# Performance work log

Measured on AMD Instinct MI355X. Metric: run time of the kernel, lower is better.

Reference implementation:

```python
import jax, jax.numpy as jnp
import numpy as np
from jax import lax

COND, PRED, DH, NOUT = 64, 32, 128, 1
M, LQ, N, LR = 8, 256, 64, 512


def setup_inputs() -> dict:
    key = jax.random.key(0)
    ks = jax.random.split(key, 8)
    g = lambda k, sh, s=0.05: jax.random.normal(k, sh, jnp.float32) * s
    return {
        "query": jax.random.normal(ks[0], (M, LQ), jnp.float32),
        "ref": jax.random.normal(ks[1], (N, LR), jnp.float32),
        "q_weight": g(ks[2], (DH, 1, COND)),
        "q_bias": jnp.zeros((DH,), jnp.float32),
        "k_weight": g(ks[3], (DH, 1, COND)),
        "k_bias": jnp.zeros((DH,), jnp.float32),
        "v_weight": g(ks[4], (DH, 1, PRED), 0.1),
        "v_bias": jnp.zeros((DH,), jnp.float32),
        "m_weight": jnp.full((NOUT, 1, COND), 1.0 / COND, jnp.float32),
        "m_bias": jnp.zeros((NOUT,), jnp.float32),
        "o_weight": g(ks[5], (NOUT * PRED, DH), 0.1),
        "o_bias": jnp.zeros((NOUT * PRED,), jnp.float32),
        "m_key": g(ks[6], (1, 1, DH), 1.0),
    }


DN = ('NCH', 'OIH', 'NCH')


def _minmax_conv(x, w, b, offset=None, scale=None):
    # x: [B,1,L], w: [H,1,k] -> y: [B,H,W]. Each length-k window is min-max
    # normalized before the conv contraction. Since offset/scale are constant
    # per window: conv((x-off)/sc) = (conv(x) - off*sum(w)) / sc.
    k = w.shape[-1]
    if offset is None:
        offset = lax.reduce_window(x, jnp.inf, lax.min, (1, 1, k), (1, 1, 1), 'VALID')
    if scale is None:
        mx = lax.reduce_window(x, -jnp.inf, lax.max, (1, 1, k), (1, 1, 1), 'VALID')
        scale = mx - offset
        scale = jnp.where(scale == 0.0, 1.0, scale)
    raw = lax.conv_general_dilated(x, w, (1,), 'VALID', dimension_numbers=DN)
    wsum = w.sum(axis=(1, 2))
    y = (raw - offset * wsum[None, :, None]) / scale + b[None, :, None]
    return y, offset, scale


def reference(query, ref, q_weight, q_bias, k_weight, k_bias, v_weight, v_bias,
              m_weight, m_bias, o_weight, o_bias, m_key):
    cond, pred = q_weight.shape[-1], v_weight.shape[-1]
    # ---- query encoding ----
    q_in = jnp.cumsum(query, axis=1)[:, None, :]
    q, q_off, q_scale = _minmax_conv(q_in, q_weight, q_bias)
    q = q.transpose(0, 2, 1)                   # [M,Q,H]
    Qn = q.shape[1]
    q_scale_t = q_scale.transpose(0, 2, 1)     # [M,Q,1]
    qp = jnp.pad(query, ((0, 0), (cond - 1, 0)))[:, None, :]
    mc = lax.conv_general_dilated(qp, m_weight, (1,), 'VALID', dimension_numbers=DN)
    mc = mc + m_bias[None, :, None]
    mc = mc[..., cond - pred:]                 # [M,NOUT,Q+pred-1]
    widx = jnp.arange(pred)[:, None] + jnp.arange(Qn)[None, :]
    mwin = mc[..., widx]                       # [M,NOUT,pred,Q]
    m = mwin.reshape(mwin.shape[0], -1, Qn).transpose(0, 2, 1)  # [M,Q,NOUT*pred]
    m = m / q_scale_t
    # ---- key / value encoding ----
    k_in = jnp.cumsum(ref, axis=1)[:, None, :-pred]
    k, k_off, k_scale = _minmax_conv(k_in, k_weight, k_bias)
    k = k.transpose(0, 2, 1)                   # [N,K,H]
    v_in = ref[:, None, cond:]
    v, _, _ = _minmax_conv(v_in, v_weight, v_bias,
                           offset=jnp.zeros_like(k_off), scale=k_scale)
    v = v.transpose(0, 2, 1)                   # [N,K,H]
    # ---- scores ----
    full_score = jnp.einsum('mqh,nkh->mqkn', q, k)           # [M,Q,K,N]
    m_score = jnp.sum(q * m_key, axis=-1, keepdims=True)     # [M,Q,1]
    # ---- semi-hard attention: top-1 window per reference series ----
    ref_score = full_score.max(axis=2)         # [M,Q,N]
    max_idx = full_score.argmax(axis=2)        # [M,Q,N]
    n_ids = jnp.arange(v.shape[0])[None, None, :]
    sel_v = v[n_ids, max_idx]                  # [M,Q,N,H]
    sel_v = sel_v @ o_weight.T + o_bias        # [M,Q,N,D]
    scores = jax.nn.softmax(jnp.concatenate([ref_score, m_score], axis=-1), axis=-1)
    rs, ms = scores[..., :-1], scores[..., -1:]
    p = jnp.einsum('mqn,mqnd->mqd', rs, sel_v) + ms * m      # [M,Q,D]
    return p * q_scale_t
```

## Files before the change

kernel.cpp:

```cpp
#include <hip/hip_runtime.h>
#include <cmath>

#define M_B   8
#define LQ    256
#define N_B   64
#define LR    512
#define COND  64
#define PRED  32
#define DH    128
#define QN    193
#define KN    417
#define QPAD  256
#define KPAD  448

typedef _Float16 half8 __attribute__((ext_vector_type(8)));
typedef float f32x16 __attribute__((ext_vector_type(16)));

__device__ __forceinline__ f32x16 mfma_f16(half8 a, half8 b, f32x16 c) {
    return __builtin_amdgcn_mfma_f32_32x32x16_f16(a, b, c, 0, 0, 0);
}
__device__ __forceinline__ f32x16 zero16() {
    f32x16 z;
    #pragma unroll
    for (int i = 0; i < 16; i++) z[i] = 0.f;
    return z;
}

#define GLOAD_LDS16(g, l) __builtin_amdgcn_global_load_lds( \
    (const __attribute__((address_space(1))) void*)(g), \
    (__attribute__((address_space(3))) void*)(l), 16, 0, 0)

#define PIN_V(x) asm volatile("" : "+v"(x))

__launch_bounds__(256, 2)
__global__ void kA_feat(const float* __restrict__ query, const float* __restrict__ ref,
                        const float* __restrict__ qw, const float* __restrict__ qb,
                        const float* __restrict__ kw, const float* __restrict__ kb,
                        const float* __restrict__ vw, const float* __restrict__ vb,
                        float* __restrict__ q_scale, float* __restrict__ qfeat,
                        _Float16* __restrict__ qg,
                        _Float16* __restrict__ kg, float* __restrict__ vfeat) {
    __shared__ float x[512];
    __shared__ float s[512];
    __shared__ float P[256];
    __shared__ float buf[128 * 65];
    const int t = threadIdx.x;
    const int kl = t & 63;
    const int hq = __builtin_amdgcn_readfirstlane(t >> 6);

    if (blockIdx.x < 448) {
        const int n = blockIdx.x / 7, chunk = blockIdx.x % 7;
        x[t] = ref[n * 512 + t];
        x[t + 256] = ref[n * 512 + t + 256];
        __syncthreads();
        P[t] = x[2 * t] + x[2 * t + 1];
        __syncthreads();
        for (int off = 1; off < 256; off <<= 1) {
            float v = (t >= off) ? P[t - off] : 0.f;
            __syncthreads();
            P[t] += v;
            __syncthreads();
        }
        s[2 * t + 1] = P[t];
        s[2 * t]     = P[t] - x[2 * t + 1];
        __syncthreads();

        const int kp = chunk * 64 + kl;
        const bool vkp = kp < KN;
        float csw[64];
        float mn = INFINITY, mx = -INFINITY;
        #pragma unroll
        for (int j = 0; j < 64; j++) {
            float v = s[kp + j];
            csw[j] = v;
            mn = fminf(mn, v);
            mx = fmaxf(mx, v);
        }
        float scv = mx - mn; if (scv == 0.f) scv = 1.f;
        const float inv = 1.f / scv;
        #pragma unroll
        for (int j = 0; j < 64; j++) { csw[j] -= mn; PIN_V(csw[j]); }

        for (int hh = 0; hh < 32; hh++) {
            const int h = hq * 32 + hh;
            const float* wrow = kw + h * 64;
            float a0 = 0.f, a1 = 0.f, a2 = 0.f, a3 = 0.f;
            #pragma unroll
            for (int j = 0; j < 64; j += 4) {
                a0 = fmaf(wrow[j],     csw[j],     a0);
                a1 = fmaf(wrow[j + 1], csw[j + 1], a1);
                a2 = fmaf(wrow[j + 2], csw[j + 2], a2);
                a3 = fmaf(wrow[j + 3], csw[j + 3], a3);
            }
            float kraw = (a0 + a1) + (a2 + a3);
            float kval = vkp ? kraw * inv + kb[h] : 0.f;
            buf[h * 65 + (kl ^ (h >> 3))] = kval;
        }
        __syncthreads();
        {
            const size_t nb = ((size_t)n * KPAD + chunk * 64) * 256;
            #pragma unroll
            for (int r = 0; r < 8; r++) {
                int task = r * 256 + t;
                int kp_l = task >> 5, g = task & 31;
                int cb = g & 15, lo = g >> 4;
                half8 hv;
                #pragma unroll
                for (int jj = 0; jj < 8; jj++) {
                    float v = buf[(cb * 8 + jj) * 65 + (kp_l ^ cb)];
                    _Float16 hi = (_Float16)v;
                    hv[jj] = lo ? (_Float16)((v - (float)hi) * 1024.0f) : hi;
                }
                *(half8*)&kg[nb + (size_t)kp_l * 256 + ((size_t)(g ^ (kp_l & 31)) << 3)] = hv;
            }
        }
        __syncthreads();
        float refw[32];
        #pragma unroll
        for (int j = 0; j < 32; j++) {
            int ri = 64 + kp + j;
            refw[j] = (ri < 512) ? x[ri] : 0.f;
            PIN_V(refw[j]);
        }
        for (int hh = 0; hh < 32; hh++) {
            const int h = hq * 32 + hh;
            const float* vrow = vw + h * 32;
            float b0 = 0.f, b1 = 0.f;
            #pragma unroll
            for (int j = 0; j < 32; j += 2) {
                b0 = fmaf(vrow[j],     refw[j],     b0);
                b1 = fmaf(vrow[j + 1], refw[j + 1], b1);
            }
            float vval = vkp ? (b0 + b1) * inv + vb[h] : 0.f;
            buf[h * 65 + (kl ^ (h >> 3))] = vval;
        }
        __syncthreads();
        {
            const size_t vb0 = ((size_t)n * KPAD + chunk * 64) * 128;
            #pragma unroll
            for (int r = 0; r < 8; r++) {
                int idx = r * 256 + t;
                int kp_l = idx >> 5, c4 = idx & 31;
                float4 o;
                o.x = buf[(c4 * 4 + 0) * 65 + (kp_l ^ ((c4 * 4 + 0) >> 3))];
                o.y = buf[(c4 * 4 + 1) * 65 + (kp_l ^ ((c4 * 4 + 1) >> 3))];
                o.z = buf[(c4 * 4 + 2) * 65 + (kp_l ^ ((c4 * 4 + 2) >> 3))];
                o.w = buf[(c4 * 4 + 3) * 65 + (kp_l ^ ((c4 * 4 + 3) >> 3))];
                *(float4*)&vfeat[vb0 + (size_t)kp_l * 128 + c4 * 4] = o;
            }
        }
    } else {
        const int id = blockIdx.x - 448;
        const int m = id >> 2, qc = id & 3;
        s[t] = query[m * 256 + t];
        __syncthreads();
        for (int off = 1; off < 256; off <<= 1) {
            float v = (t >= off) ? s[t - off] : 0.f;
            __syncthreads();
            s[t] += v;
            __syncthreads();
        }
        const int qpos = qc * 64 + kl;
        const bool vq = qpos < QN;
        const int base = vq ? qpos : (QN - 1);
        float csw[64];
        float mn = INFINITY, mx = -INFINITY;
        #pragma unroll
        for (int j = 0; j < 64; j++) {
            float v = s[base + j];
            csw[j] = v;
            mn = fminf(mn, v);
            mx = fmaxf(mx, v);
        }
        float sc = mx - mn; if (sc == 0.f) sc = 1.f;
        const float inv = 1.f / sc;
        if (t < 64) q_scale[m * QPAD + qpos] = vq ? sc : 1.f;
        #pragma unroll
        for (int j = 0; j < 64; j++) { csw[j] -= mn; PIN_V(csw[j]); }

        for (int hh = 0; hh < 32; hh++) {
            const int h = hq * 32 + hh;
            const float* wrow = qw + h * 64;
            float a0 = 0.f, a1 = 0.f, a2 = 0.f, a3 = 0.f;
            #pragma unroll
            for (int j = 0; j < 64; j += 4) {
                a0 = fmaf(wrow[j],     csw[j],     a0);
                a1 = fmaf(wrow[j + 1], csw[j + 1], a1);
                a2 = fmaf(wrow[j + 2], csw[j + 2], a2);
                a3 = fmaf(wrow[j + 3], csw[j + 3], a3);
            }
            float raw = (a0 + a1) + (a2 + a3);
            float val = vq ? raw * inv + qb[h] : 0.f;
            buf[h * 65 + (kl ^ (h >> 3))] = val;
        }
        __syncthreads();
        const size_t qb0 = ((size_t)m * QPAD + qc * 64) * 128;
        #pragma unroll
        for (int r = 0; r < 8; r++) {
            int idx = r * 256 + t;
            int qp_l = idx >> 5, c4 = idx & 31;
            float4 o;
            o.x = buf[(c4 * 4 + 0) * 65 + (qp_l ^ ((c4 * 4 + 0) >> 3))];
            o.y = buf[(c4 * 4 + 1) * 65 + (qp_l ^ ((c4 * 4 + 1) >> 3))];
            o.z = buf[(c4 * 4 + 2) * 65 + (qp_l ^ ((c4 * 4 + 2) >> 3))];
            o.w = buf[(c4 * 4 + 3) * 65 + (qp_l ^ ((c4 * 4 + 3) >> 3))];
            *(float4*)&qfeat[qb0 + (size_t)qp_l * 128 + c4 * 4] = o;
        }
        #pragma unroll
        for (int r = 0; r < 8; r++) {
            int idx = r * 256 + t;
            int qp_l = idx >> 5, g = idx & 31;
            int c = g >> 2, kh = (g >> 1) & 1, lo = g & 1;
            half8 hv;
            #pragma unroll
            for (int jj = 0; jj < 8; jj++) {
                int h = c * 16 + kh * 8 + jj;
                float v = buf[h * 65 + (qp_l ^ (h >> 3))];
                _Float16 hi = (_Float16)v;
                hv[jj] = lo ? (_Float16)((v - (float)hi) * 1024.0f) : hi;
            }
            int qp2 = qc * 64 + qp_l;
            int grp = (m << 3) | (qp2 >> 5);
            size_t fb = (size_t)(grp * 16 + c * 2 + lo);
            *(half8*)&qg[fb * 512 + (size_t)(kh * 32 + (qp2 & 31)) * 8] = hv;
        }
    }
}

__launch_bounds__(256, 2)
__global__ void k3_score(const _Float16* __restrict__ qg, const _Float16* __restrict__ kg,
                         float* __restrict__ bscore, int* __restrict__ bidx) {
    __shared__ _Float16 Kbuf[2][32 * 256];
    const int blk = blockIdx.x;
    const int n = blk & 63, qt = blk >> 6;
    const int t = threadIdx.x, w = t >> 6, l = t & 63;
    const int lrow = l & 31, khalf = l >> 5;

    half8 qf[2][8][2];
    #pragma unroll
    for (int r = 0; r < 2; r++) {
        const int grp = (qt * 4 + w) * 2 + r;
        #pragma unroll
        for (int c = 0; c < 8; c++)
            #pragma unroll
            for (int h = 0; h < 2; h++)
                qf[r][c][h] = ((const half8*)qg)[(size_t)(grp * 16 + c * 2 + h) * 64 + l];
    }

    const _Float16* ksrc = kg + (size_t)n * KPAD * 256;

    float best[2][16];
    unsigned bkt[4] = {0u, 0u, 0u, 0u};
    #pragma unroll
    for (int r = 0; r < 2; r++)
        #pragma unroll
        for (int g = 0; g < 16; g++) best[r][g] = -INFINITY;

    #pragma unroll
    for (int rd = 0; rd < 4; rd++) {
        int e = (rd * 4 + w) * 512 + l * 8;
        GLOAD_LDS16(ksrc + e, &Kbuf[0][0] + e);
    }

    for (int kt = 0; kt < 14; kt++) {
        __syncthreads();
        if (kt < 13) {
            const _Float16* src = ksrc + (size_t)(kt + 1) * (32 * 256);
            _Float16* dst = &Kbuf[(kt + 1) & 1][0];
            #pragma unroll
            for (int rd = 0; rd < 4; rd++) {
                int e = (rd * 4 + w) * 512 + l * 8;
                GLOAD_LDS16(src + e, dst + e);
            }
        }
        const _Float16* kb = &Kbuf[kt & 1][0];
        f32x16 accH[2], accL[2];
        accH[0] = zero16(); accH[1] = zero16();
        accL[0] = zero16(); accL[1] = zero16();
        #pragma unroll
        for (int c = 0; c < 8; c++) {
            half8 bh = *(const half8*)(kb + lrow * 256 + (((c * 2 + khalf) ^ lrow) * 8));
            half8 bl = *(const half8*)(kb + lrow * 256 + (((16 + c * 2 + khalf) ^ lrow) * 8));
            #pragma unroll
            for (int r = 0; r < 2; r++) {
                accH[r] = mfma_f16(qf[r][c][0], bh, accH[r]);
                accL[r] = mfma_f16(qf[r][c][0], bl, accL[r]);
                accL[r] = mfma_f16(qf[r][c][1], bh, accL[r]);
            }
        }
        const int kp = kt * 32 + lrow;
        const bool valid = kp < KN;
        #pragma unroll
        for (int r = 0; r < 2; r++) {
            #pragma unroll
            for (int g = 0; g < 16; g++) {
                float sv = fmaf(accL[r][g], 0.0009765625f, accH[r][g]);
                if (valid && (sv > best[r][g])) {
                    best[r][g] = sv;
                    const int slot = r * 16 + g;
                    const unsigned sh = (unsigned)(slot & 7) * 4u;
                    bkt[slot >> 3] = (bkt[slot >> 3] & ~(0xFu << sh)) | ((unsigned)kt << sh);
                }
            }
        }
    }

    #pragma unroll
    for (int r = 0; r < 2; r++) {
        #pragma unroll
        for (int g = 0; g < 16; g++) {
            float sv = best[r][g];
            const int slot = r * 16 + g;
            int ktb = (int)((bkt[slot >> 3] >> ((slot & 7) * 4)) & 0xFu);
            int kp = ktb * 32 + lrow;
            for (int msk = 1; msk < 32; msk <<= 1) {
                float os = __shfl_xor(sv, msk, 64);
                int okp = __shfl_xor(kp, msk, 64);
                if (os > sv || (os == sv && okp < kp)) { sv = os; kp = okp; }
            }
            if (lrow == 0) {
                int row = (g & 3) + 8 * (g >> 2) + 4 * khalf;
                int mq = (qt * 4 + w) * 64 + r * 32 + row;
                if ((mq & 255) < QN) {
                    bscore[(size_t)mq * 64 + n] = sv;
                    bidx[(size_t)mq * 64 + n] = kp;
                }
            }
        }
    }
}

__global__ void k4_out(const float* __restrict__ query,
                       const float* __restrict__ qfeat, const float* __restrict__ vfeat,
                       const float* __restrict__ bscore, const int* __restrict__ bidx,
                       const float* __restrict__ q_scale,
                       const float* __restrict__ mw, const float* __restrict__ mb,
                       const float* __restrict__ mkey,
                       const float* __restrict__ ow, const float* __restrict__ ob,
                       float* __restrict__ out) {
    __shared__ float rsS[4][64];
    __shared__ int   idxS[4][64];
    __shared__ float wS[4][128];
    const int t = threadIdx.x, wv = t >> 6, l = t & 63;
    const int j = blockIdx.x * 4 + wv;
    const int m = j / QN, qpos = j - m * QN;
    const int mq = m * QPAD + qpos;

    float s = bscore[(size_t)mq * 64 + l];
    int idx = bidx[(size_t)mq * 64 + l];
    float msv = qfeat[(size_t)mq * 128 + l] * mkey[l]
              + qfeat[(size_t)mq * 128 + 64 + l] * mkey[64 + l];
    #pragma unroll
    for (int msk = 1; msk < 64; msk <<= 1) msv += __shfl_xor(msv, msk, 64);
    float mx = s;
    #pragma unroll
    for (int msk = 1; msk < 64; msk <<= 1) mx = fmaxf(mx, __shfl_xor(mx, msk, 64));
    mx = fmaxf(mx, msv);
    float e = expf(s - mx);
    float sum = e;
    #pragma unroll
    for (int msk = 1; msk < 64; msk <<= 1) sum += __shfl_xor(sum, msk, 64);
    float ems = expf(msv - mx);
    float inv = 1.f / (sum + ems);
    float rs = e * inv, msw = ems * inv;

    rsS[wv][l] = rs; idxS[wv][l] = idx;
    __syncthreads();
    float ax = 0.f, ay = 0.f;
    #pragma unroll 8
    for (int nn = 0; nn < 64; nn++) {
        float r = rsS[wv][nn];
        int id = idxS[wv][nn];
        const float2 v = *(const float2*)&vfeat[((size_t)nn * KPAD + id) * 128 + 2 * l];
        ax = fmaf(r, v.x, ax);
        ay = fmaf(r, v.y, ay);
    }
    wS[wv][2 * l] = ax; wS[wv][2 * l + 1] = ay;
    __syncthreads();
    if (l < 32) {
        float p = 0.f;
        #pragma unroll
        for (int h4 = 0; h4 < 32; h4++) {
            const float4 wv4 = *(const float4*)&wS[wv][h4 * 4];
            const float4 o4 = *(const float4*)&ow[l * 128 + h4 * 4];
            p += wv4.x * o4.x + wv4.y * o4.y + wv4.z * o4.z + wv4.w * o4.w;
        }
        p += (1.f - msw) * ob[l];
        float mcv = mb[0];
        const int tpos = 32 + qpos + l;
        for (int jj = 0; jj < 64; jj++) {
            int qi = tpos + jj - 63;
            if (qi >= 0) mcv = fmaf(mw[jj], query[m * 256 + qi], mcv);
        }
        float outv = q_scale[mq] * p + msw * mcv;
        out[(size_t)j * 32 + l] = outv;
    }
}

extern "C" void kernel_launch(void* const* d_in, const int* in_sizes, int n_in,
                              void* d_out, int out_size, void* d_ws, size_t ws_size,
                              hipStream_t stream) {
    const float* query = (const float*)d_in[0];
    const float* ref   = (const float*)d_in[1];
    const float* qw    = (const float*)d_in[2];
    const float* qb    = (const float*)d_in[3];
    const float* kw    = (const float*)d_in[4];
    const float* kb    = (const float*)d_in[5];
    const float* vw    = (const float*)d_in[6];
    const float* vb    = (const float*)d_in[7];
    const float* mw    = (const float*)d_in[8];
    const float* mb    = (const float*)d_in[9];
    const float* ow    = (const float*)d_in[10];
    const float* ob    = (const float*)d_in[11];
    const float* mkey  = (const float*)d_in[12];
    float* out = (float*)d_out;

    float* ws = (float*)d_ws;
    float* q_scale = ws;
    float* qfeat   = ws + 2048;
    float* bscore  = ws + 264192;
    int*   bidx    = (int*)(ws + 395264);
    _Float16* qg   = (_Float16*)(ws + 526336);
    _Float16* kg   = (_Float16*)(ws + 788480);
    float* vfeat   = ws + 4458496;

    hipLaunchKernelGGL(kA_feat, dim3(480), dim3(256), 0, stream,
                       query, ref, qw, qb, kw, kb, vw, vb,
                       q_scale, qfeat, qg, kg, vfeat);
    hipLaunchKernelGGL(k3_score, dim3(512), dim3(256), 0, stream,
                       qg, kg, bscore, bidx);
    hipLaunchKernelGGL(k4_out, dim3(386), dim3(256), 0, stream,
                       query, qfeat, vfeat, bscore, bidx, q_scale, mw, mb, mkey, ow, ob, out);
}
```

Before: 200.1 us.

## Use wave-shuffle prefix scans and deepen K prefetch to a 4-buffer pipeline

Replaces the LDS Hillis-Steele prefix sums in the feature kernel with wavefront shuffle scans plus a cross-wave offset pass, removing many block-wide barriers. In the score kernel, K tiles move from a double buffer to a 4-slot ring prefetched two tiles ahead. Manual vmcnt waits and raw s_barrier replace __syncthreads, so loads stay in flight across iterations. This raises LDS use of the score kernel to 64KB, which may limit occupancy, and relies on hand-counted vmcnt values being correct.

```diff
diff --git a/kernel.cpp b/kernel.cpp
--- a/kernel.cpp
+++ b/kernel.cpp
@@ -42,27 +42,33 @@
                         _Float16* __restrict__ kg, float* __restrict__ vfeat) {
     __shared__ float x[512];
     __shared__ float s[512];
-    __shared__ float P[256];
+    __shared__ float wtot[4];
     __shared__ float buf[128 * 65];
     const int t = threadIdx.x;
     const int kl = t & 63;
+    const int lane = t & 63, wv = t >> 6;
     const int hq = __builtin_amdgcn_readfirstlane(t >> 6);
 
     if (blockIdx.x < 448) {
         const int n = blockIdx.x / 7, chunk = blockIdx.x % 7;
-        x[t] = ref[n * 512 + t];
-        x[t + 256] = ref[n * 512 + t + 256];
-        __syncthreads();
-        P[t] = x[2 * t] + x[2 * t + 1];
-        __syncthreads();
-        for (int off = 1; off < 256; off <<= 1) {
-            float v = (t >= off) ? P[t - off] : 0.f;
-            __syncthreads();
-            P[t] += v;
-            __syncthreads();
-        }
-        s[2 * t + 1] = P[t];
-        s[2 * t]     = P[t] - x[2 * t + 1];
+        const float2 pr = *(const float2*)&ref[n * 512 + 2 * t];
+        const float a = pr.x, b = pr.y;
+        const float ls = a + b;
+        float sc = ls;
+        #pragma unroll
+        for (int d = 1; d < 64; d <<= 1) {
+            float v = __shfl_up(sc, d, 64);
+            if (lane >= d) sc += v;
+        }
+        if (lane == 63) wtot[wv] = sc;
+        x[2 * t] = a; x[2 * t + 1] = b;
+        __syncthreads();
+        float woff = 0.f;
+        #pragma unroll
+        for (int w2 = 0; w2 < 3; w2++) if (w2 < wv) woff += wtot[w2];
+        const float excl = woff + sc - ls;
+        s[2 * t] = excl + a;
+        s[2 * t + 1] = excl + a + b;
         __syncthreads();
 
         const int kp = chunk * 64 + kl;
@@ -152,14 +158,21 @@
     } else {
         const int id = blockIdx.x - 448;
         const int m = id >> 2, qc = id & 3;
-        s[t] = query[m * 256 + t];
-        __syncthreads();
-        for (int off = 1; off < 256; off <<= 1) {
-            float v = (t >= off) ? s[t - off] : 0.f;
-            __syncthreads();
-            s[t] += v;
-            __syncthreads();
-        }
+        const float a = query[m * 256 + t];
+        float sc = a;
+        #pragma unroll
+        for (int d = 1; d < 64; d <<= 1) {
+            float v = __shfl_up(sc, d, 64);
+            if (lane >= d) sc += v;
+        }
+        if (lane == 63) wtot[wv] = sc;
+        __syncthreads();
+        float woff = 0.f;
+        #pragma unroll
+        for (int w2 = 0; w2 < 3; w2++) if (w2 < wv) woff += wtot[w2];
+        s[t] = woff + sc;
+        __syncthreads();
+
         const int qpos = qc * 64 + kl;
         const bool vq = qpos < QN;
         const int base = vq ? qpos : (QN - 1);
@@ -172,9 +185,9 @@
             mn = fminf(mn, v);
             mx = fmaxf(mx, v);
         }
-        float sc = mx - mn; if (sc == 0.f) sc = 1.f;
-        const float inv = 1.f / sc;
-        if (t < 64) q_scale[m * QPAD + qpos] = vq ? sc : 1.f;
+        float sq = mx - mn; if (sq == 0.f) sq = 1.f;
+        const float inv = 1.f / sq;
+        if (t < 64) q_scale[m * QPAD + qpos] = vq ? sq : 1.f;
         #pragma unroll
         for (int j = 0; j < 64; j++) { csw[j] -= mn; PIN_V(csw[j]); }
 
@@ -230,7 +243,7 @@
 __launch_bounds__(256, 2)
 __global__ void k3_score(const _Float16* __restrict__ qg, const _Float16* __restrict__ kg,
                          float* __restrict__ bscore, int* __restrict__ bidx) {
-    __shared__ _Float16 Kbuf[2][32 * 256];
+    __shared__ _Float16 Kbuf[4][32 * 256];
     const int blk = blockIdx.x;
     const int n = blk & 63, qt = blk >> 6;
     const int t = threadIdx.x, w = t >> 6, l = t & 63;
@@ -261,19 +274,30 @@
         int e = (rd * 4 + w) * 512 + l * 8;
         GLOAD_LDS16(ksrc + e, &Kbuf[0][0] + e);
     }
+    #pragma unroll
+    for (int rd = 0; rd < 4; rd++) {
+        int e = (rd * 4 + w) * 512 + l * 8;
+        GLOAD_LDS16(ksrc + 32 * 256 + e, &Kbuf[1][0] + e);
+    }
 
     for (int kt = 0; kt < 14; kt++) {
-        __syncthreads();
-        if (kt < 13) {
-            const _Float16* src = ksrc + (size_t)(kt + 1) * (32 * 256);
-            _Float16* dst = &Kbuf[(kt + 1) & 1][0];
+        if (kt < 12) {
+            const _Float16* src = ksrc + (size_t)(kt + 2) * (32 * 256);
+            _Float16* dst = &Kbuf[(kt + 2) & 3][0];
             #pragma unroll
             for (int rd = 0; rd < 4; rd++) {
                 int e = (rd * 4 + w) * 512 + l * 8;
                 GLOAD_LDS16(src + e, dst + e);
             }
-        }
-        const _Float16* kb = &Kbuf[kt & 1][0];
+            asm volatile("s_waitcnt vmcnt(8)" ::: "memory");
+        } else if (kt == 12) {
+            asm volatile("s_waitcnt vmcnt(4)" ::: "memory");
+        } else {
+            asm volatile("s_waitcnt vmcnt(0)" ::: "memory");
+        }
+        asm volatile("s_barrier" ::: "memory");
+
+        const _Float16* kb = &Kbuf[kt & 3][0];
         f32x16 accH[2], accL[2];
         accH[0] = zero16(); accH[1] = zero16();
         accL[0] = zero16(); accL[1] = zero16();
```

New measurement: 200.3 us. About the same (+0.1%).
